# Optimization experiments

Measured on AMD Instinct MI355X. Metric: run time of the kernel, lower is better.

## Reference

```python
import jax, jax.numpy as jnp
import numpy as np

N_E = 1024
E_DIM = 256
BETA = 0.25
EPS = 1e-10


def setup_inputs() -> dict:
    key = jax.random.key(0)
    k1, k2 = jax.random.split(key)
    z = jax.random.normal(k1, (32, E_DIM, 32, 32), dtype=jnp.float32)
    emb = jax.random.normal(k2, (N_E, E_DIM), dtype=jnp.float32)
    return {"z": z, "emb": emb}


def reference(z, emb):
    sg = jax.lax.stop_gradient
    # (B, C, H, W) -> (B, H, W, C)
    zp = jnp.transpose(z, (0, 2, 3, 1))
    zf = zp.reshape(-1, E_DIM)  # (N, C), N = B*H*W
    # squared euclidean distances: ||z||^2 + ||e||^2 - 2 z e^T  -> (N, n_e)
    d = (jnp.sum(zf * zf, axis=1, keepdims=True)
         + jnp.sum(emb * emb, axis=1)
         - 2.0 * jnp.matmul(zf, emb.T))
    idx = jnp.argmin(d, axis=1)  # (N,)
    # one-hot @ codebook == gather (same math, no dense one-hot matmul)
    z_q1 = emb[idx].reshape(zp.shape)  # (B, H, W, C)
    # loss: note original does NOT detach z_q1 anywhere
    loss = jnp.mean((z_q1 - zp) ** 2) + BETA * jnp.mean((z_q1 - sg(zp)) ** 2)
    # straight-through (original detaches z, not z_q1)
    z_q = zp + (z_q1 - sg(zp))
    # perplexity from mean one-hot encodings = normalized histogram of indices
    counts = jnp.bincount(idx, length=N_E)
    e_mean = counts.astype(zf.dtype) / idx.shape[0]
    perplexity = jnp.exp(-jnp.sum(e_mean * jnp.log(e_mean + EPS)))
    z_q = jnp.transpose(z_q, (0, 3, 1, 2))
    z_q1_out = jnp.transpose(z_q1, (0, 3, 1, 2))
    return loss, z_q, perplexity, idx, z_q1_out
```

## Files before the change

### kernel.cpp

```cpp
#include <hip/hip_runtime.h>
#include <hip/hip_bf16.h>
#include <math.h>

#define CDIM 256
#define HW   1024
#define NVEC 32768
#define NE   1024
#define ZSIZE 8388608
#define NSPLIT 2
#define MARGIN 0.05f

#define OUT_LOSS 0
#define OUT_ZQ   1
#define OUT_PERP 8388609
#define OUT_IDX  8388610
#define OUT_ZQ1  8421378

#define WS_LOSS   0
#define WS_RCNT   64
#define WS_HIST   128
#define WS_ENORM  4224
#define WS_IDX    8448
#define WS_RLIST  139520
#define WS_S1     270592
#define WS_S2     532736
#define WS_J1     794880
#define WS_EBH    1057024
#define WS_EBL    1581312
#define WS_ZBH    2105600
#define WS_ZBL    18882816

typedef __attribute__((ext_vector_type(8))) short short8;
typedef __attribute__((ext_vector_type(4))) float f32x4;
typedef __attribute__((ext_vector_type(8))) unsigned short ushort8v;

__device__ __forceinline__ unsigned short bf16_rne(float x) {
    union { float f; unsigned u; } v; v.f = x;
    unsigned r = v.u + 0x7FFFu + ((v.u >> 16) & 1u);
    return (unsigned short)(r >> 16);
}
__device__ __forceinline__ float bf16_to_f(unsigned short h) {
    union { unsigned u; float f; } v; v.u = ((unsigned)h) << 16;
    return v.f;
}
__device__ __forceinline__ void lds_barrier() {
    asm volatile("s_waitcnt lgkmcnt(0)\n\ts_barrier" ::: "memory");
}

__global__ __launch_bounds__(256) void vq_prep(
    const float* __restrict__ z, const float* __restrict__ emb,
    unsigned short* __restrict__ zbh, unsigned short* __restrict__ zbl,
    unsigned short* __restrict__ ebh, unsigned short* __restrict__ ebl,
    float* __restrict__ enorm)
{
    const int tid = threadIdx.x, w = tid >> 6, L = tid & 63;
    if (blockIdx.x < 512) {
        __shared__ unsigned short th[64 * 264];
        __shared__ unsigned short tl[64 * 264];
        const int b = blockIdx.x >> 4, hw0 = (blockIdx.x & 15) << 6;
        const float* zp = z + (size_t)b * (CDIM * HW) + hw0;
        for (int i = 0; i < 16; ++i) {
            int k = (i * 4 + w) * 4;
            float f0 = zp[(size_t)(k + 0) * HW + L];
            float f1 = zp[(size_t)(k + 1) * HW + L];
            float f2 = zp[(size_t)(k + 2) * HW + L];
            float f3 = zp[(size_t)(k + 3) * HW + L];
            ushort4 hi = { bf16_rne(f0), bf16_rne(f1), bf16_rne(f2), bf16_rne(f3) };
            ushort4 lo = { bf16_rne(f0 - bf16_to_f(hi.x)), bf16_rne(f1 - bf16_to_f(hi.y)),
                           bf16_rne(f2 - bf16_to_f(hi.z)), bf16_rne(f3 - bf16_to_f(hi.w)) };
            *(ushort4*)&th[L * 264 + k] = hi;
            *(ushort4*)&tl[L * 264 + k] = lo;
        }
        __syncthreads();
#pragma unroll
        for (int it = 0; it < 8; ++it) {
            int row = it * 8 + (tid >> 5);
            int kc = (tid & 31) * 8;
            size_t o = (size_t)(b * 1024 + hw0 + row) * CDIM + kc;
            *(ushort8v*)(zbh + o) = *(ushort8v*)&th[row * 264 + kc];
            *(ushort8v*)(zbl + o) = *(ushort8v*)&tl[row * 264 + kc];
        }
    } else {
        const int cb = (int)(blockIdx.x - 512) * 64;
        for (int p = 0; p < 16; ++p) {
            int code = cb + p * 4 + w;
            float4 v = *(const float4*)(emb + (size_t)code * CDIM + L * 4);
            float s = v.x * v.x + v.y * v.y + v.z * v.z + v.w * v.w;
            for (int off = 32; off; off >>= 1) s += __shfl_down(s, off, 64);
            if (L == 0) enorm[code] = s;
            ushort4 hi = { bf16_rne(v.x), bf16_rne(v.y), bf16_rne(v.z), bf16_rne(v.w) };
            ushort4 lo = { bf16_rne(v.x - bf16_to_f(hi.x)), bf16_rne(v.y - bf16_to_f(hi.y)),
                           bf16_rne(v.z - bf16_to_f(hi.z)), bf16_rne(v.w - bf16_to_f(hi.w)) };
            *(ushort4*)(ebh + (size_t)code * CDIM + L * 4) = hi;
            *(ushort4*)(ebl + (size_t)code * CDIM + L * 4) = lo;
        }
    }
}

__global__ __launch_bounds__(256, 2) void vq_mfma3(
    const unsigned short* __restrict__ zbh, const unsigned short* __restrict__ zbl,
    const unsigned short* __restrict__ ebh, const unsigned short* __restrict__ ebl,
    const float* __restrict__ enorm,
    float* __restrict__ s1_ws, float* __restrict__ s2_ws, int* __restrict__ j1_ws)
{
    __shared__ short albuf[32768];
    __shared__ short bbuf[8192];

    const int tid = threadIdx.x, w = tid >> 6, L = tid & 63;
    const int l15 = L & 15, q = L >> 4;
    const int r16 = tid & 15, ch = (tid >> 4) & 3;
    const int mtile = blockIdx.x & 255, js = blockIdx.x >> 8;
    const int n0 = mtile << 7;
    const int jsbase = js << 9;

#pragma unroll
    for (int ro = 0; ro < 16; ++ro) {
        const int seg = ro * 4 + w;
        const int sw2 = seg >> 4, smf = (seg >> 3) & 1, skk = seg & 7;
        short8 v = *(const short8*)(zbl + (size_t)(n0 + sw2 * 32 + smf * 16 + r16) * CDIM + skk * 32 + ch * 8);
        *(short8*)(albuf + seg * 512 + L * 8) = v;
    }
    short8 AH[2][8];
#pragma unroll
    for (int mf = 0; mf < 2; ++mf)
#pragma unroll
        for (int kk = 0; kk < 8; ++kk)
            AH[mf][kk] = *(const short8*)(zbh + (size_t)(n0 + w * 32 + mf * 16 + l15) * CDIM + kk * 32 + q * 8);
    __syncthreads();

    float s1[2][4], s2[2][4]; int j1[2][4];
#pragma unroll
    for (int mf = 0; mf < 2; ++mf)
#pragma unroll
        for (int r = 0; r < 4; ++r) { s1[mf][r] = -3.4e38f; s2[mf][r] = -3.4e38f; j1[mf][r] = 0; }

    for (int j0i = 0; j0i < 4; ++j0i) {
        const int j0 = jsbase + j0i * 128;
        f32x4 acc[2][8] = {};
        short8 st[4];
#pragma unroll
        for (int ro = 0; ro < 4; ++ro) {
            const unsigned short* src = (ro >= 2) ? ebl : ebh;
            const int jf = (ro & 1) * 4 + w;
            st[ro] = *(const short8*)(src + (size_t)(j0 + jf * 16 + r16) * CDIM + ch * 8);
        }
#pragma unroll
        for (int kk = 0; kk < 8; ++kk) {
            lds_barrier();
#pragma unroll
            for (int ro = 0; ro < 4; ++ro)
                *(short8*)(bbuf + (ro * 4 + w) * 512 + L * 8) = st[ro];
            if (kk < 7) {
                const int k0n = (kk + 1) * 32;
#pragma unroll
                for (int ro = 0; ro < 4; ++ro) {
                    const unsigned short* src = (ro >= 2) ? ebl : ebh;
                    const int jf = (ro & 1) * 4 + w;
                    st[ro] = *(const short8*)(src + (size_t)(j0 + jf * 16 + r16) * CDIM + k0n + ch * 8);
                }
            }
            lds_barrier();
            short8 AL0 = *(const short8*)(albuf + (w * 16 + kk) * 512 + L * 8);
            short8 AL1 = *(const short8*)(albuf + (w * 16 + 8 + kk) * 512 + L * 8);
#pragma unroll
            for (int jf = 0; jf < 8; ++jf) {
                short8 Bh = *(const short8*)(bbuf + jf * 512 + L * 8);
                short8 Bl = *(const short8*)(bbuf + (8 + jf) * 512 + L * 8);
                acc[0][jf] = __builtin_amdgcn_mfma_f32_16x16x32_bf16(AH[0][kk], Bh, acc[0][jf], 0, 0, 0);
                acc[1][jf] = __builtin_amdgcn_mfma_f32_16x16x32_bf16(AH[1][kk], Bh, acc[1][jf], 0, 0, 0);
                acc[0][jf] = __builtin_amdgcn_mfma_f32_16x16x32_bf16(AH[0][kk], Bl, acc[0][jf], 0, 0, 0);
                acc[1][jf] = __builtin_amdgcn_mfma_f32_16x16x32_bf16(AH[1][kk], Bl, acc[1][jf], 0, 0, 0);
                acc[0][jf] = __builtin_amdgcn_mfma_f32_16x16x32_bf16(AL0, Bh, acc[0][jf], 0, 0, 0);
                acc[1][jf] = __builtin_amdgcn_mfma_f32_16x16x32_bf16(AL1, Bh, acc[1][jf], 0, 0, 0);
            }
        }
#pragma unroll
        for (int jf = 0; jf < 8; ++jf) {
            const int j = j0 + jf * 16 + l15;
            const float hn = 0.5f * enorm[j];
#pragma unroll
            for (int mf = 0; mf < 2; ++mf)
#pragma unroll
                for (int r = 0; r < 4; ++r) {
                    float s = acc[mf][jf][r] - hn;
                    if (s > s1[mf][r]) { s2[mf][r] = s1[mf][r]; s1[mf][r] = s; j1[mf][r] = j; }
                    else if (s > s2[mf][r]) s2[mf][r] = s;
                }
        }
    }

#pragma unroll
    for (int mf = 0; mf < 2; ++mf)
#pragma unroll
        for (int r = 0; r < 4; ++r) {
            float a1 = s1[mf][r], a2 = s2[mf][r]; int aj = j1[mf][r];
            for (int m = 1; m < 16; m <<= 1) {
                float o1 = __shfl_xor(a1, m, 64);
                float o2 = __shfl_xor(a2, m, 64);
                int   oj = __shfl_xor(aj, m, 64);
                if (o1 > a1 || (o1 == a1 && oj < aj)) { a2 = fmaxf(a1, o2); a1 = o1; aj = oj; }
                else a2 = fmaxf(a2, o1);
            }
            if (l15 == 0) {
                int o = js * NVEC + n0 + w * 32 + mf * 16 + q * 4 + r;
                s1_ws[o] = a1; s2_ws[o] = a2; j1_ws[o] = aj;
            }
        }
}

__global__ __launch_bounds__(256) void vq_merge(
    const float* __restrict__ s1_ws, const float* __restrict__ s2_ws,
    const int* __restrict__ j1_ws, int* __restrict__ idx_ws,
    float* __restrict__ idx_out, int* __restrict__ hist,
    int* __restrict__ rcnt, int* __restrict__ rlist)
{
    int n = blockIdx.x * 256 + threadIdx.x;
    float b1 = -3.4e38f, b2 = -3.4e38f; int bj = 0;
#pragma unroll
    for (int s = 0; s < NSPLIT; ++s) {
        float a1 = s1_ws[s * NVEC + n], a2 = s2_ws[s * NVEC + n];
        int aj = j1_ws[s * NVEC + n];
        if (a1 > b1 || (a1 == b1 && aj < bj)) { b2 = fmaxf(b1, a2); b1 = a1; bj = aj; }
        else b2 = fmaxf(b2, a1);
    }
    idx_ws[n] = bj;
    if (b1 - b2 < MARGIN) {
        int p = atomicAdd(rcnt, 1); rlist[p] = n;
    } else {
        idx_out[n] = (float)bj;
        atomicAdd(&hist[bj], 1);
    }
}

__global__ __launch_bounds__(256) void vq_rescue(
    const float* __restrict__ z, const float* __restrict__ emb,
    const float* __restrict__ enorm, const int* __restrict__ rcnt,
    const int* __restrict__ rlist, int* __restrict__ idx_ws,
    float* __restrict__ idx_out, int* __restrict__ hist)
{
    __shared__ __align__(16) float zrow[256];
    __shared__ float rs[256];
    __shared__ int   rj[256];
    const int tid = threadIdx.x;
    const int count = *rcnt;

    for (int it = blockIdx.x; it < count; it += gridDim.x) {
        __syncthreads();
        int n = rlist[it];
        zrow[tid] = z[(size_t)(n >> 10) * (CDIM * HW) + (size_t)tid * HW + (n & 1023)];
        __syncthreads();

        const float* er0 = emb + (size_t)(tid      ) * CDIM;
        const float* er1 = emb + (size_t)(tid + 256) * CDIM;
        const float* er2 = emb + (size_t)(tid + 512) * CDIM;
        const float* er3 = emb + (size_t)(tid + 768) * CDIM;
        float s0 = 0.f, sA = 0.f, sB = 0.f, sC = 0.f;
#pragma unroll 4
        for (int kc = 0; kc < 256; kc += 4) {
            float4 zv = *(const float4*)&zrow[kc];
            float4 e0 = *(const float4*)(er0 + kc);
            float4 e1 = *(const float4*)(er1 + kc);
            float4 e2 = *(const float4*)(er2 + kc);
            float4 e3 = *(const float4*)(er3 + kc);
            s0 = fmaf(zv.x, e0.x, s0); s0 = fmaf(zv.y, e0.y, s0);
            s0 = fmaf(zv.z, e0.z, s0); s0 = fmaf(zv.w, e0.w, s0);
            sA = fmaf(zv.x, e1.x, sA); sA = fmaf(zv.y, e1.y, sA);
            sA = fmaf(zv.z, e1.z, sA); sA = fmaf(zv.w, e1.w, sA);
            sB = fmaf(zv.x, e2.x, sB); sB = fmaf(zv.y, e2.y, sB);
            sB = fmaf(zv.z, e2.z, sB); sB = fmaf(zv.w, e2.w, sB);
            sC = fmaf(zv.x, e3.x, sC); sC = fmaf(zv.y, e3.y, sC);
            sC = fmaf(zv.z, e3.z, sC); sC = fmaf(zv.w, e3.w, sC);
        }
        s0 -= 0.5f * enorm[tid];
        sA -= 0.5f * enorm[tid + 256];
        sB -= 0.5f * enorm[tid + 512];
        sC -= 0.5f * enorm[tid + 768];
        float b1 = s0; int bj = tid;
        if (sA > b1) { b1 = sA; bj = tid + 256; }
        if (sB > b1) { b1 = sB; bj = tid + 512; }
        if (sC > b1) { b1 = sC; bj = tid + 768; }
        rs[tid] = b1; rj[tid] = bj;
        __syncthreads();
        for (int step = 128; step >= 1; step >>= 1) {
            if (tid < step) {
                float so = rs[tid + step]; int jo = rj[tid + step];
                if (so > rs[tid] || (so == rs[tid] && jo < rj[tid])) { rs[tid] = so; rj[tid] = jo; }
            }
            __syncthreads();
        }
        if (tid == 0) {
            idx_ws[n] = rj[0];
            idx_out[n] = (float)rj[0];
            atomicAdd(&hist[rj[0]], 1);
        }
    }
}

__global__ __launch_bounds__(256) void vq_gather(
    const float* __restrict__ z, const float* __restrict__ emb,
    const int* __restrict__ idx_ws, float* __restrict__ zq,
    float* __restrict__ zq1, double* __restrict__ loss_sum)
{
    __shared__ float es[32 * 129];
    __shared__ int ids[32];
    __shared__ float wred[4];

    const int tid = threadIdx.x, w = tid >> 6, L = tid & 63;
    const int b   = blockIdx.x >> 6;
    const int half = (blockIdx.x >> 5) & 1;
    const int hw0 = (blockIdx.x & 31) << 5;
    const int n0  = (b << 10) + hw0;
    const int c0  = half << 7;

    if (tid < 32) ids[tid] = idx_ws[n0 + tid];
    __syncthreads();

#pragma unroll
    for (int p = 0; p < 4; ++p) {
        int u = p * 256 + tid;
        int r = u >> 5, cq = (u & 31) * 4;
        float4 v = *(const float4*)(emb + (size_t)ids[r] * CDIM + c0 + cq);
        es[r * 129 + cq + 0] = v.x;
        es[r * 129 + cq + 1] = v.y;
        es[r * 129 + cq + 2] = v.z;
        es[r * 129 + cq + 3] = v.w;
    }
    __syncthreads();

    const int row = L & 31, cp = L >> 5;
    const size_t zbase = (size_t)b * (CDIM * HW) + hw0 + row;
    float ls = 0.f;
    for (int rd = 0; rd < 16; ++rd) {
        int cl = rd * 8 + w * 2 + cp;
        size_t off = zbase + (size_t)(c0 + cl) * HW;
        float zv = z[off];
        float e  = es[row * 129 + cl];
        float d  = e - zv;
        zq[off]  = zv + d;
        zq1[off] = e;
        ls += d * d;
    }

    for (int off = 32; off; off >>= 1) ls += __shfl_down(ls, off, 64);
    if (L == 0) wred[w] = ls;
    __syncthreads();
    if (tid == 0)
        atomicAdd(loss_sum, (double)(wred[0] + wred[1] + wred[2] + wred[3]));
}

__global__ __launch_bounds__(1024) void vq_final(
    const int* __restrict__ hist, const double* __restrict__ loss_sum,
    float* __restrict__ out_loss, float* __restrict__ out_perp)
{
    int tid = threadIdx.x;
    float em = (float)hist[tid] * (1.0f / 32768.0f);
    float term = em * logf(em + 1e-10f);
    for (int off = 32; off; off >>= 1) term += __shfl_down(term, off, 64);
    __shared__ float red[16];
    int lane = tid & 63, wv = tid >> 6;
    if (lane == 0) red[wv] = term;
    __syncthreads();
    if (tid == 0) {
        float s = 0.f;
        for (int i = 0; i < 16; ++i) s += red[i];
        *out_perp = expf(-s);
        *out_loss = (float)(*loss_sum * 1.25 / 8388608.0);
    }
}

extern "C" void kernel_launch(void* const* d_in, const int* in_sizes, int n_in,
                              void* d_out, int out_size, void* d_ws, size_t ws_size,
                              hipStream_t stream) {
    const float* z   = (const float*)d_in[0];
    const float* emb = (const float*)d_in[1];
    float* out = (float*)d_out;
    char*  ws  = (char*)d_ws;

    double* loss_sum    = (double*)(ws + WS_LOSS);
    int*    rcnt        = (int*)(ws + WS_RCNT);
    int*    hist        = (int*)(ws + WS_HIST);
    float*  enorm       = (float*)(ws + WS_ENORM);
    int*    idx_ws      = (int*)(ws + WS_IDX);
    int*    rlist       = (int*)(ws + WS_RLIST);
    float*  s1_ws       = (float*)(ws + WS_S1);
    float*  s2_ws       = (float*)(ws + WS_S2);
    int*    j1_ws       = (int*)(ws + WS_J1);
    unsigned short* ebh = (unsigned short*)(ws + WS_EBH);
    unsigned short* ebl = (unsigned short*)(ws + WS_EBL);
    unsigned short* zbh = (unsigned short*)(ws + WS_ZBH);
    unsigned short* zbl = (unsigned short*)(ws + WS_ZBL);

    hipMemsetAsync(d_ws, 0, 4224, stream);

    vq_prep  <<<528, 256, 0, stream>>>(z, emb, zbh, zbl, ebh, ebl, enorm);
    vq_mfma3 <<<512, 256, 0, stream>>>(zbh, zbl, ebh, ebl, enorm, s1_ws, s2_ws, j1_ws);
    vq_merge <<<128, 256, 0, stream>>>(s1_ws, s2_ws, j1_ws, idx_ws, out + OUT_IDX, hist, rcnt, rlist);
    vq_rescue<<<512, 256, 0, stream>>>(z, emb, enorm, rcnt, rlist, idx_ws, out + OUT_IDX, hist);
    vq_gather<<<2048, 256, 0, stream>>>(z, emb, idx_ws, out + OUT_ZQ, out + OUT_ZQ1, loss_sum);
    vq_final <<<1, 1024, 0, stream>>>(hist, loss_sum, out + OUT_LOSS, out + OUT_PERP);
}
```

Baseline: 275.3 us.

## Rework rescue kernel to coalesced per-wave codebook dot products with shuffle reductions

```diff
diff --git a/kernel.cpp b/kernel.cpp
--- a/kernel.cpp
+++ b/kernel.cpp
@@ -239,59 +239,56 @@
     float* __restrict__ idx_out, int* __restrict__ hist)
 {
     __shared__ __align__(16) float zrow[256];
-    __shared__ float rs[256];
-    __shared__ int   rj[256];
+    __shared__ float rs[4];
+    __shared__ int   rj[4];
     const int tid = threadIdx.x;
+    const int wv = tid >> 6, L = tid & 63;
     const int count = *rcnt;
 
     for (int it = blockIdx.x; it < count; it += gridDim.x) {
         __syncthreads();
-        int n = rlist[it];
+        const int n = rlist[it];
         zrow[tid] = z[(size_t)(n >> 10) * (CDIM * HW) + (size_t)tid * HW + (n & 1023)];
         __syncthreads();
-
-        const float* er0 = emb + (size_t)(tid      ) * CDIM;
-        const float* er1 = emb + (size_t)(tid + 256) * CDIM;
-        const float* er2 = emb + (size_t)(tid + 512) * CDIM;
-        const float* er3 = emb + (size_t)(tid + 768) * CDIM;
-        float s0 = 0.f, sA = 0.f, sB = 0.f, sC = 0.f;
+        const float4 zv = *(const float4*)&zrow[L * 4];
+
+        float b1 = -3.4e38f; int bj = 0x7fffffff;
+        const int jbase = wv << 8;
+        const int jodd = L >> 5;
 #pragma unroll 4
-        for (int kc = 0; kc < 256; kc += 4) {
-            float4 zv = *(const float4*)&zrow[kc];
-            float4 e0 = *(const float4*)(er0 + kc);
-            float4 e1 = *(const float4*)(er1 + kc);
-            float4 e2 = *(const float4*)(er2 + kc);
-            float4 e3 = *(const float4*)(er3 + kc);
-            s0 = fmaf(zv.x, e0.x, s0); s0 = fmaf(zv.y, e0.y, s0);
-            s0 = fmaf(zv.z, e0.z, s0); s0 = fmaf(zv.w, e0.w, s0);
-            sA = fmaf(zv.x, e1.x, sA); sA = fmaf(zv.y, e1.y, sA);
-            sA = fmaf(zv.z, e1.z, sA); sA = fmaf(zv.w, e1.w, sA);
-            sB = fmaf(zv.x, e2.x, sB); sB = fmaf(zv.y, e2.y, sB);
-            sB = fmaf(zv.z, e2.z, sB); sB = fmaf(zv.w, e2.w, sB);
-            sC = fmaf(zv.x, e3.x, sC); sC = fmaf(zv.y, e3.y, sC);
-            sC = fmaf(zv.z, e3.z, sC); sC = fmaf(zv.w, e3.w, sC);
-        }
-        s0 -= 0.5f * enorm[tid];
-        sA -= 0.5f * enorm[tid + 256];
-        sB -= 0.5f * enorm[tid + 512];
-        sC -= 0.5f * enorm[tid + 768];
-        float b1 = s0; int bj = tid;
-        if (sA > b1) { b1 = sA; bj = tid + 256; }
-        if (sB > b1) { b1 = sB; bj = tid + 512; }
-        if (sC > b1) { b1 = sC; bj = tid + 768; }
-        rs[tid] = b1; rj[tid] = bj;
+        for (int jo = 0; jo < 256; jo += 2) {
+            const int jA = jbase + jo;
+            const float4 eA = *(const float4*)(emb + (size_t)jA * CDIM + L * 4);
+            const float4 eB = *(const float4*)(emb + (size_t)(jA + 1) * CDIM + L * 4);
+            float pA = fmaf(zv.x, eA.x, fmaf(zv.y, eA.y, fmaf(zv.z, eA.z, zv.w * eA.w)));
+            float pB = fmaf(zv.x, eB.x, fmaf(zv.y, eB.y, fmaf(zv.z, eB.z, zv.w * eB.w)));
+            float tA = pA + __shfl_xor(pA, 32, 64);
+            float tB = pB + __shfl_xor(pB, 32, 64);
+            float u = (L < 32) ? tA : tB;
+            u += __shfl_xor(u, 16, 64);
+            u += __shfl_xor(u, 8, 64);
+            u += __shfl_xor(u, 4, 64);
+            u += __shfl_xor(u, 2, 64);
+            u += __shfl_xor(u, 1, 64);
+            const int j = jA + jodd;
+            const float s = u - 0.5f * enorm[j];
+            if (s > b1 || (s == b1 && j < bj)) { b1 = s; bj = j; }
+        }
+        {
+            const float o1 = __shfl_xor(b1, 32, 64);
+            const int   oj = __shfl_xor(bj, 32, 64);
+            if (o1 > b1 || (o1 == b1 && oj < bj)) { b1 = o1; bj = oj; }
+        }
+        if (L == 0) { rs[wv] = b1; rj[wv] = bj; }
         __syncthreads();
-        for (int step = 128; step >= 1; step >>= 1) {
-            if (tid < step) {
-                float so = rs[tid + step]; int jo = rj[tid + step];
-                if (so > rs[tid] || (so == rs[tid] && jo < rj[tid])) { rs[tid] = so; rj[tid] = jo; }
-            }
-            __syncthreads();
-        }
         if (tid == 0) {
-            idx_ws[n] = rj[0];
-            idx_out[n] = (float)rj[0];
-            atomicAdd(&hist[rj[0]], 1);
+            float f1 = rs[0]; int fj = rj[0];
+#pragma unroll
+            for (int v = 1; v < 4; ++v)
+                if (rs[v] > f1 || (rs[v] == f1 && rj[v] < fj)) { f1 = rs[v]; fj = rj[v]; }
+            idx_ws[n] = fj;
+            idx_out[n] = (float)fj;
+            atomicAdd(&hist[fj], 1);
         }
     }
 }
```

After: 277.5 us. About the same (+0.8%).
